# Kernel tuning notes

Hardware: AMD Instinct MI355X
Metric: run time of the kernel (lower is better)

The kernel has to match this reference:

```python
import jax, jax.numpy as jnp
import numpy as np

N = 50000       # num nodes
F_IN = 256      # num_features
HID = 128       # num_hidden
E = 800000      # structural edges (no self loops)
E_KNN = 500000  # knn edges (no self loops)


def setup_inputs() -> dict:
    rng = np.random.default_rng(0)
    # loop-free random edges: col != row guaranteed
    row = rng.integers(0, N, E)
    col = (row + 1 + rng.integers(0, N - 1, E)) % N
    edge_index = jnp.asarray(np.stack([row, col]), dtype=jnp.int32)
    rowk = rng.integers(0, N, E_KNN)
    colk = (rowk + 1 + rng.integers(0, N - 1, E_KNN)) % N
    knn_graph = jnp.asarray(np.stack([rowk, colk]), dtype=jnp.int32)

    key = jax.random.key(0)
    ks = jax.random.split(key, 8)
    x = jax.random.normal(ks[0], (N, F_IN), dtype=jnp.float32)
    s = 1.0 / np.sqrt(F_IN)  # nn.Linear default init range
    def lin(kw, kb):
        W = jax.random.uniform(kw, (HID, F_IN), minval=-s, maxval=s, dtype=jnp.float32)
        b = jax.random.uniform(kb, (HID,), minval=-s, maxval=s, dtype=jnp.float32)
        return W, b
    W_s1, b_s1 = lin(ks[1], ks[2])
    W_s2, b_s2 = lin(ks[3], ks[4])
    W_f2, b_f2 = lin(ks[5], ks[6])
    return {"x": x, "edge_index": edge_index, "knn_graph": knn_graph,
            "W_s1": W_s1, "b_s1": b_s1, "W_s2": W_s2, "b_s2": b_s2,
            "W_f2": W_f2, "b_f2": b_f2}


def _gcn_norm(edge_index, num_nodes):
    # add_remaining_self_loops on loop-free input == append all self loops (w=1)
    loop = jnp.arange(num_nodes, dtype=edge_index.dtype)
    row = jnp.concatenate([edge_index[0], loop])
    col = jnp.concatenate([edge_index[1], loop])
    w = jnp.ones(row.shape[0], dtype=jnp.float32)
    deg = jax.ops.segment_sum(w, col, num_segments=num_nodes)
    dinv = jnp.where(deg > 0, jax.lax.rsqrt(deg), 0.0)
    return row, col, dinv[row] * w * dinv[col]


def _gcn(x, W, b, row, col, norm, K):
    # eval mode: dropout(p=0.6) is identity
    h = x @ W.T + b
    n = x.shape[0]
    for _ in range(K):
        # gather source feats -> edge-weight scale -> scatter-add to targets (SpMM)
        h = jax.ops.segment_sum(norm[:, None] * h[row], col, num_segments=n)
    return h


def reference(x, edge_index, knn_graph, W_s1, b_s1, W_s2, b_s2, W_f2, b_f2):
    n = x.shape[0]
    r, c, nm = _gcn_norm(edge_index, n)
    rk, ck, nmk = _gcn_norm(knn_graph, n)
    h0 = _gcn(x, W_s1, b_s1, r, c, nm, 2)
    h1 = _gcn(x, W_s2, b_s2, r, c, nm, 10)
    z0 = _gcn(x, W_f2, b_f2, r, c, nm, 2)
    # original computes gcn_f2(x, edge_index, K=2) twice; in eval mode both equal z0
    z1 = z0 + _gcn(x, W_f2, b_f2, rk, ck, nmk, 1)
    return (h0, h1, z0, z1)
```

## Files before the change

kernel.cpp:

```cpp
#include <hip/hip_runtime.h>
#include <hip/hip_fp16.h>

#define F_IN 256
#define HID 128

typedef _Float16 half8 __attribute__((ext_vector_type(8)));
typedef _Float16 half4v __attribute__((ext_vector_type(4)));
typedef float f32x4 __attribute__((ext_vector_type(4)));


__global__ void k_count2(const int* __restrict__ col_s, int E, int* __restrict__ cnt_s,
                         const int* __restrict__ col_k, int EK, int* __restrict__ cnt_k) {
  int e = blockIdx.x * blockDim.x + threadIdx.x;
  if (e < E) {
    atomicAdd(&cnt_s[col_s[e]], 1);
  } else {
    int f = e - E;
    if (f < EK) atomicAdd(&cnt_k[col_k[f]], 1);
  }
}

__global__ void k_scan_block(const int* __restrict__ in, int n, int* __restrict__ out,
                             int* __restrict__ bsum) {
  __shared__ int s[1024];
  int tid = threadIdx.x;
  int i = blockIdx.x * 1024 + tid;
  int v = (i < n) ? in[i] : 0;
  s[tid] = v;
  __syncthreads();
  for (int off = 1; off < 1024; off <<= 1) {
    int t = (tid >= off) ? s[tid - off] : 0;
    __syncthreads();
    s[tid] += t;
    __syncthreads();
  }
  if (i < n) out[i] = s[tid] - v;
  if (tid == 1023) bsum[blockIdx.x] = s[1023];
}

__global__ void k_scan_single(int* __restrict__ bsum, int nb, int* __restrict__ tail) {
  if (threadIdx.x == 0 && blockIdx.x == 0) {
    int run = 0;
    for (int b = 0; b < nb; ++b) { int t = bsum[b]; bsum[b] = run; run += t; }
    *tail = run;
  }
}

__global__ void k_add_off(int* __restrict__ out, const int* __restrict__ bsum, int n) {
  int i = blockIdx.x * blockDim.x + threadIdx.x;
  if (i < n) out[i] += bsum[i >> 10];
}

__global__ void k_scatter2(const int* __restrict__ row_s, const int* __restrict__ col_s, int E,
                           const int* __restrict__ offs_s, int* __restrict__ cur_s,
                           int* __restrict__ csr_s,
                           const int* __restrict__ row_k, const int* __restrict__ col_k, int EK,
                           const int* __restrict__ offs_k, int* __restrict__ cur_k,
                           int* __restrict__ csr_k) {
  int e = blockIdx.x * blockDim.x + threadIdx.x;
  if (e < E) {
    int c = col_s[e];
    int p = offs_s[c] + atomicAdd(&cur_s[c], 1);
    csr_s[p] = row_s[e];
  } else {
    int f = e - E;
    if (f < EK) {
      int c = col_k[f];
      int p = offs_k[c] + atomicAdd(&cur_k[c], 1);
      csr_k[p] = row_k[f];
    }
  }
}


__global__ void k_cvt_w(const float* __restrict__ W0, const float* __restrict__ W1,
                        const float* __restrict__ W2, _Float16* __restrict__ Wh) {
  const int sz = HID * F_IN;
  int idx = (blockIdx.x * 256 + threadIdx.x) * 4;
  const float* src = (idx < sz) ? (W0 + idx)
                   : (idx < 2 * sz) ? (W1 + idx - sz)
                   : (W2 + idx - 2 * sz);
  float4 v = *(const float4*)src;
  half4v o;
  o[0] = (_Float16)v.x; o[1] = (_Float16)v.y; o[2] = (_Float16)v.z; o[3] = (_Float16)v.w;
  *(half4v*)(Wh + idx) = o;
}


__global__ __launch_bounds__(256, 8) void k_gemm3(
    const float* __restrict__ x, const _Float16* __restrict__ Wh,
    const float* __restrict__ b0, const float* __restrict__ b1, const float* __restrict__ b2,
    int n, const int* __restrict__ cnt_s, const int* __restrict__ cnt_k,
    _Float16* __restrict__ gS1, _Float16* __restrict__ gS2,
    _Float16* __restrict__ gF2s, _Float16* __restrict__ gF2k)
{
  __shared__ _Float16 xs[32 * F_IN];
  int tid = threadIdx.x;
  int m0 = blockIdx.x * 32;

  {
    int r = tid >> 3;
    int cbase = (tid & 7) * 32;
    int gr = m0 + r; if (gr >= n) gr = n - 1;
    const float* src = x + (size_t)gr * F_IN + cbase;
    unsigned sw = (unsigned)((r & 7) << 4);
    char* drow = (char*)xs + r * (F_IN * 2);
#pragma unroll
    for (int i = 0; i < 4; ++i) {
      float4 a = *(const float4*)(src + i * 8);
      float4 b = *(const float4*)(src + i * 8 + 4);
      half8 v;
      v[0] = (_Float16)a.x; v[1] = (_Float16)a.y; v[2] = (_Float16)a.z; v[3] = (_Float16)a.w;
      v[4] = (_Float16)b.x; v[5] = (_Float16)b.y; v[6] = (_Float16)b.z; v[7] = (_Float16)b.w;
      *(half8*)(drow + (((unsigned)(cbase * 2 + i * 16)) ^ sw)) = v;
    }
  }
  __syncthreads();

  int lane = tid & 63;
  int wv = tid >> 6;
  int mh = wv >> 1, ch = wv & 1;
  int l15 = lane & 15, lhi = lane >> 4;
  int rloc = mh * 16 + l15;
  unsigned swr = (unsigned)((rloc & 7) << 4);
  const char* xrow = (const char*)xs + rloc * (F_IN * 2);

  int node = m0 + rloc;
  int cn = (node < n) ? node : (n - 1);
  float ss = rsqrtf((float)(cnt_s[cn] + 1));
  float sk = rsqrtf((float)(cnt_k[cn] + 1));

#pragma unroll 1
  for (int w = 0; w < 3; ++w) {
    const float* bias = (w == 0) ? b0 : (w == 1) ? b1 : b2;
    _Float16* dst = (w == 0) ? gS1 : (w == 1) ? gS2 : gF2s;
    const _Float16* Wp = Wh + (size_t)w * HID * F_IN
                            + (size_t)(ch * 64 + l15) * F_IN + lhi * 8;

    f32x4 acc[4];
#pragma unroll
    for (int nt = 0; nt < 4; ++nt) {
      float4 bv = *(const float4*)(bias + ch * 64 + nt * 16 + lhi * 4);
      acc[nt] = (f32x4){bv.x, bv.y, bv.z, bv.w};
    }

#pragma unroll
    for (int kt = 0; kt < 8; ++kt) {
      half8 xf = *(const half8*)(xrow + (((unsigned)((kt * 32 + lhi * 8) * 2)) ^ swr));
#pragma unroll
      for (int nt = 0; nt < 4; ++nt) {
        half8 wf = *(const half8*)(Wp + (size_t)nt * 16 * F_IN + kt * 32);
        acc[nt] = __builtin_amdgcn_mfma_f32_16x16x32_f16(wf, xf, acc[nt], 0, 0, 0);
      }
    }

    if (node < n) {
      size_t obase = (size_t)node * HID + ch * 64 + lhi * 4;
#pragma unroll
      for (int nt = 0; nt < 4; ++nt) {
        half4v o;
        o[0] = (_Float16)(acc[nt][0] * ss); o[1] = (_Float16)(acc[nt][1] * ss);
        o[2] = (_Float16)(acc[nt][2] * ss); o[3] = (_Float16)(acc[nt][3] * ss);
        *(half4v*)(dst + obase + nt * 16) = o;
      }
      if (w == 2) {
#pragma unroll
        for (int nt = 0; nt < 4; ++nt) {
          half4v o2;
          o2[0] = (_Float16)(acc[nt][0] * sk); o2[1] = (_Float16)(acc[nt][1] * sk);
          o2[2] = (_Float16)(acc[nt][2] * sk); o2[3] = (_Float16)(acc[nt][3] * sk);
          *(half4v*)(gF2k + obase + nt * 16) = o2;
        }
      }
    }
  }
}


__device__ inline float2 h2f2(unsigned int u) {
  __half2 h; *(unsigned int*)&h = u; return __half22float2(h);
}

__device__ inline void spmm_store(void* out, size_t base, float2 acc, float deg, int mode,
                                  const float2* __restrict__ add) {
  if (mode == 0) {
    float sc = 1.0f / deg;
    __half2 h = __float22half2_rn(make_float2(acc.x * sc, acc.y * sc));
    ((__half2*)out)[base] = h;
  } else {
    float sc = rsqrtf(deg);
    float2 o = make_float2(acc.x * sc, acc.y * sc);
    if (mode == 2) { float2 z = add[base]; o.x += z.x; o.y += z.y; }
    ((float2*)out)[base] = o;
  }
}

__global__ __launch_bounds__(256) void k_spmm_h(
    const unsigned int* __restrict__ gin, void* __restrict__ gout,
    const int* __restrict__ csr, const int* __restrict__ offs, const int* __restrict__ cnt,
    int n, int mode, const float2* __restrict__ addsrc)
{
  int w = (blockIdx.x << 2) | ((int)threadIdx.x >> 6);
  if (w >= n) return;
  int lane = threadIdx.x & 63;
  int beg = offs[w], end = offs[w + 1];
  size_t base = (size_t)w * 64 + lane;
  float2 acc = h2f2(gin[base]);
  int e = beg;
#pragma unroll 1
  for (; e + 16 <= end; e += 16) {
    unsigned int u[16];
#pragma unroll
    for (int j = 0; j < 16; ++j)
      u[j] = gin[((size_t)(unsigned)csr[e + j] << 6) + lane];
    float sx = 0.f, sy = 0.f;
#pragma unroll
    for (int j = 0; j < 16; ++j) { float2 v = h2f2(u[j]); sx += v.x; sy += v.y; }
    acc.x += sx; acc.y += sy;
  }
#pragma unroll 1
  for (; e + 4 <= end; e += 4) {
    unsigned int u[4];
#pragma unroll
    for (int j = 0; j < 4; ++j)
      u[j] = gin[((size_t)(unsigned)csr[e + j] << 6) + lane];
    float sx = 0.f, sy = 0.f;
#pragma unroll
    for (int j = 0; j < 4; ++j) { float2 v = h2f2(u[j]); sx += v.x; sy += v.y; }
    acc.x += sx; acc.y += sy;
  }
  for (; e < end; ++e) {
    float2 v = h2f2(gin[((size_t)(unsigned)csr[e] << 6) + lane]);
    acc.x += v.x; acc.y += v.y;
  }
  spmm_store(gout, base, acc, (float)(cnt[w] + 1), mode, addsrc);
}

__global__ __launch_bounds__(256) void k_spmm3(
    const unsigned int* __restrict__ g0, const unsigned int* __restrict__ g1,
    const unsigned int* __restrict__ g2,
    void* __restrict__ o0, void* __restrict__ o1, void* __restrict__ o2,
    int md0, int md1, int md2,
    const int* __restrict__ csr, const int* __restrict__ offs, const int* __restrict__ cnt,
    int n)
{
  int w = (blockIdx.x << 2) | ((int)threadIdx.x >> 6);
  if (w >= n) return;
  int lane = threadIdx.x & 63;
  int beg = offs[w], end = offs[w + 1];
  size_t base = (size_t)w * 64 + lane;
  float2 a0 = h2f2(g0[base]), a1 = h2f2(g1[base]), a2 = h2f2(g2[base]);
  int e = beg;
#pragma unroll 1
  for (; e + 4 <= end; e += 4) {
    size_t s[4];
#pragma unroll
    for (int j = 0; j < 4; ++j) s[j] = ((size_t)(unsigned)csr[e + j] << 6) + lane;
    unsigned int u0[4], u1[4], u2[4];
#pragma unroll
    for (int j = 0; j < 4; ++j) { u0[j] = g0[s[j]]; u1[j] = g1[s[j]]; u2[j] = g2[s[j]]; }
#pragma unroll
    for (int j = 0; j < 4; ++j) {
      float2 v;
      v = h2f2(u0[j]); a0.x += v.x; a0.y += v.y;
      v = h2f2(u1[j]); a1.x += v.x; a1.y += v.y;
      v = h2f2(u2[j]); a2.x += v.x; a2.y += v.y;
    }
  }
  for (; e < end; ++e) {
    size_t s0 = ((size_t)(unsigned)csr[e] << 6) + lane;
    float2 v;
    v = h2f2(g0[s0]); a0.x += v.x; a0.y += v.y;
    v = h2f2(g1[s0]); a1.x += v.x; a1.y += v.y;
    v = h2f2(g2[s0]); a2.x += v.x; a2.y += v.y;
  }
  float deg = (float)(cnt[w] + 1);
  spmm_store(o0, base, a0, deg, md0, nullptr);
  spmm_store(o1, base, a1, deg, md1, nullptr);
  spmm_store(o2, base, a2, deg, md2, nullptr);
}


extern "C" void kernel_launch(void* const* d_in, const int* in_sizes, int n_in,
                              void* d_out, int out_size, void* d_ws, size_t ws_size,
                              hipStream_t stream) {
  const float* x    = (const float*)d_in[0];
  const int*   ei   = (const int*)d_in[1];
  const int*   knn  = (const int*)d_in[2];
  const float* W_s1 = (const float*)d_in[3];
  const float* b_s1 = (const float*)d_in[4];
  const float* W_s2 = (const float*)d_in[5];
  const float* b_s2 = (const float*)d_in[6];
  const float* W_f2 = (const float*)d_in[7];
  const float* b_f2 = (const float*)d_in[8];

  const int N  = in_sizes[0] / F_IN;
  const int E  = in_sizes[1] / 2;
  const int EK = in_sizes[2] / 2;
  const int* row_s = ei;   const int* col_s = ei + E;
  const int* row_k = knn;  const int* col_k = knn + EK;

  char* p = (char*)d_ws;
  auto carve = [&](size_t bytes) {
    char* r = p; p += (bytes + 511) & ~(size_t)511; return (void*)r;
  };
  int* cnt_s = (int*)carve((size_t)N * 4);
  int* cnt_k = (int*)carve((size_t)N * 4);
  int* cur_s = (int*)carve((size_t)N * 4);
  int* cur_k = (int*)carve((size_t)N * 4);
  char* zero_end = p;
  int* offs_s = (int*)carve((size_t)(N + 1) * 4);
  int* offs_k = (int*)carve((size_t)(N + 1) * 4);
  int* bsum   = (int*)carve(4096);
  int* csr_s  = (int*)carve((size_t)E * 4);
  int* csr_k  = (int*)carve((size_t)EK * 4);
  _Float16* Wh  = (_Float16*)carve((size_t)3 * HID * F_IN * 2);
  _Float16* gS1 = (_Float16*)carve((size_t)N * HID * 2);
  _Float16* gS2 = (_Float16*)carve((size_t)N * HID * 2);
  _Float16* gF2s= (_Float16*)carve((size_t)N * HID * 2);
  _Float16* gF2k= (_Float16*)carve((size_t)N * HID * 2);
  _Float16* tS2 = (_Float16*)carve((size_t)N * HID * 2);

  float* out_h0 = (float*)d_out;
  float* out_h1 = out_h0 + (size_t)N * HID;
  float* out_z0 = out_h1 + (size_t)N * HID;
  float* out_z1 = out_z0 + (size_t)N * HID;
  _Float16* tS1 = (_Float16*)out_z1;
  _Float16* tF2 = tS1 + (size_t)N * HID;

  hipMemsetAsync(d_ws, 0, (size_t)(zero_end - (char*)d_ws), stream);

  const int tpb = 256;
  int etot = E + EK;
  k_count2<<<(etot + tpb - 1) / tpb, tpb, 0, stream>>>(col_s, E, cnt_s, col_k, EK, cnt_k);

  int nb = (N + 1023) / 1024;
  k_scan_block<<<nb, 1024, 0, stream>>>(cnt_s, N, offs_s, bsum);
  k_scan_single<<<1, 64, 0, stream>>>(bsum, nb, offs_s + N);
  k_add_off<<<(N + tpb - 1) / tpb, tpb, 0, stream>>>(offs_s, bsum, N);
  k_scan_block<<<nb, 1024, 0, stream>>>(cnt_k, N, offs_k, bsum);
  k_scan_single<<<1, 64, 0, stream>>>(bsum, nb, offs_k + N);
  k_add_off<<<(N + tpb - 1) / tpb, tpb, 0, stream>>>(offs_k, bsum, N);

  k_scatter2<<<(etot + tpb - 1) / tpb, tpb, 0, stream>>>(
      row_s, col_s, E, offs_s, cur_s, csr_s,
      row_k, col_k, EK, offs_k, cur_k, csr_k);

  k_cvt_w<<<96, 256, 0, stream>>>(W_s1, W_s2, W_f2, Wh);
  k_gemm3<<<(N + 31) / 32, 256, 0, stream>>>(x, Wh, b_s1, b_s2, b_f2, N, cnt_s, cnt_k,
                                             gS1, gS2, gF2s, gF2k);

  int spmm_grid = (N + 3) / 4;

  k_spmm3<<<spmm_grid, 256, 0, stream>>>((const unsigned int*)gS1, (const unsigned int*)gS2,
                                         (const unsigned int*)gF2s,
                                         tS1, tS2, tF2, 0, 0, 0,
                                         csr_s, offs_s, cnt_s, N);
  k_spmm3<<<spmm_grid, 256, 0, stream>>>((const unsigned int*)tS1, (const unsigned int*)tS2,
                                         (const unsigned int*)tF2,
                                         out_h0, gS1, out_z0, 1, 0, 1,
                                         csr_s, offs_s, cnt_s, N);

  {
    _Float16* cur = gS1; _Float16* alt = tS2;
    for (int it = 0; it < 7; ++it) {
      k_spmm_h<<<spmm_grid, 256, 0, stream>>>((const unsigned int*)cur, alt,
                                              csr_s, offs_s, cnt_s, N, 0, nullptr);
      _Float16* t = cur; cur = alt; alt = t;
    }
    k_spmm_h<<<spmm_grid, 256, 0, stream>>>((const unsigned int*)cur, out_h1,
                                            csr_s, offs_s, cnt_s, N, 1, nullptr);
  }

  k_spmm_h<<<spmm_grid, 256, 0, stream>>>((const unsigned int*)gF2k, out_z1,
                                          csr_k, offs_k, cnt_k, N, 2,
                                          (const float2*)out_z0);
}
```

Measured before the change: 725.8 us.

## Vectorize SpMM gathers with 16-byte loads and split edges across lane groups

The SpMM kernels change lane mapping: each wavefront now splits into four 16-lane groups, each handling a different neighbor edge and loading 16 bytes (8 halfs) per lane instead of 4 bytes. Partial sums are combined with cross-group shuffles and only group 0 writes. The aim is fewer, wider memory transactions and more edges in flight per wave. The GEMM kernel also gains software prefetching of the next k-step's fragments and a lower launch-bounds occupancy hint. The costs are extra shuffle reductions, higher register pressure, and idle lanes on the final partial batch of edges.

```diff
diff --git a/kernel.cpp b/kernel.cpp
--- a/kernel.cpp
+++ b/kernel.cpp
@@ -7,6 +7,7 @@
 typedef _Float16 half8 __attribute__((ext_vector_type(8)));
 typedef _Float16 half4v __attribute__((ext_vector_type(4)));
 typedef float f32x4 __attribute__((ext_vector_type(4)));
+typedef unsigned int uint4v __attribute__((ext_vector_type(4)));
 
 
 __global__ void k_count2(const int* __restrict__ col_s, int E, int* __restrict__ cnt_s,
@@ -87,7 +88,7 @@
 }
 
 
-__global__ __launch_bounds__(256, 8) void k_gemm3(
+__global__ __launch_bounds__(256, 6) void k_gemm3(
     const float* __restrict__ x, const _Float16* __restrict__ Wh,
     const float* __restrict__ b0, const float* __restrict__ b1, const float* __restrict__ b2,
     int n, const int* __restrict__ cnt_s, const int* __restrict__ cnt_k,
@@ -144,13 +145,28 @@
       acc[nt] = (f32x4){bv.x, bv.y, bv.z, bv.w};
     }
 
+    half8 xf = *(const half8*)(xrow + (((unsigned)((0 * 32 + lhi * 8) * 2)) ^ swr));
+    half8 wf[4];
+#pragma unroll
+    for (int nt = 0; nt < 4; ++nt)
+      wf[nt] = *(const half8*)(Wp + (size_t)nt * 16 * F_IN + 0 * 32);
+
 #pragma unroll
     for (int kt = 0; kt < 8; ++kt) {
-      half8 xf = *(const half8*)(xrow + (((unsigned)((kt * 32 + lhi * 8) * 2)) ^ swr));
-#pragma unroll
-      for (int nt = 0; nt < 4; ++nt) {
-        half8 wf = *(const half8*)(Wp + (size_t)nt * 16 * F_IN + kt * 32);
-        acc[nt] = __builtin_amdgcn_mfma_f32_16x16x32_f16(wf, xf, acc[nt], 0, 0, 0);
+      half8 xfn; half8 wfn[4];
+      if (kt < 7) {
+        xfn = *(const half8*)(xrow + (((unsigned)(((kt + 1) * 32 + lhi * 8) * 2)) ^ swr));
+#pragma unroll
+        for (int nt = 0; nt < 4; ++nt)
+          wfn[nt] = *(const half8*)(Wp + (size_t)nt * 16 * F_IN + (kt + 1) * 32);
+      }
+#pragma unroll
+      for (int nt = 0; nt < 4; ++nt)
+        acc[nt] = __builtin_amdgcn_mfma_f32_16x16x32_f16(wf[nt], xf, acc[nt], 0, 0, 0);
+      if (kt < 7) {
+        xf = xfn;
+#pragma unroll
+        for (int nt = 0; nt < 4; ++nt) wf[nt] = wfn[nt];
       }
     }
 
@@ -181,64 +197,111 @@
   __half2 h; *(unsigned int*)&h = u; return __half22float2(h);
 }
 
-__device__ inline void spmm_store(void* out, size_t base, float2 acc, float deg, int mode,
-                                  const float2* __restrict__ add) {
-  if (mode == 0) {
-    float sc = 1.0f / deg;
-    __half2 h = __float22half2_rn(make_float2(acc.x * sc, acc.y * sc));
-    ((__half2*)out)[base] = h;
-  } else {
-    float sc = rsqrtf(deg);
-    float2 o = make_float2(acc.x * sc, acc.y * sc);
-    if (mode == 2) { float2 z = add[base]; o.x += z.x; o.y += z.y; }
-    ((float2*)out)[base] = o;
-  }
-}
-
 __global__ __launch_bounds__(256) void k_spmm_h(
-    const unsigned int* __restrict__ gin, void* __restrict__ gout,
+    const _Float16* __restrict__ gin, void* __restrict__ gout,
     const int* __restrict__ csr, const int* __restrict__ offs, const int* __restrict__ cnt,
-    int n, int mode, const float2* __restrict__ addsrc)
+    int n, int mode, const float* __restrict__ addsrc)
 {
   int w = (blockIdx.x << 2) | ((int)threadIdx.x >> 6);
   if (w >= n) return;
   int lane = threadIdx.x & 63;
+  int g = lane >> 4;
+  int c = lane & 15;
   int beg = offs[w], end = offs[w + 1];
-  size_t base = (size_t)w * 64 + lane;
-  float2 acc = h2f2(gin[base]);
+
+  float acc[8];
+#pragma unroll
+  for (int i = 0; i < 8; ++i) acc[i] = 0.f;
+
   int e = beg;
 #pragma unroll 1
   for (; e + 16 <= end; e += 16) {
-    unsigned int u[16];
-#pragma unroll
-    for (int j = 0; j < 16; ++j)
-      u[j] = gin[((size_t)(unsigned)csr[e + j] << 6) + lane];
-    float sx = 0.f, sy = 0.f;
-#pragma unroll
-    for (int j = 0; j < 16; ++j) { float2 v = h2f2(u[j]); sx += v.x; sy += v.y; }
-    acc.x += sx; acc.y += sy;
+    int idx[4];
+#pragma unroll
+    for (int j = 0; j < 4; ++j) idx[j] = csr[e + 4 * j + g];
+    uint4v u[4];
+#pragma unroll
+    for (int j = 0; j < 4; ++j)
+      u[j] = *(const uint4v*)(gin + ((size_t)(unsigned)idx[j] << 7) + c * 8);
+#pragma unroll
+    for (int j = 0; j < 4; ++j)
+#pragma unroll
+      for (int q = 0; q < 4; ++q) {
+        float2 v = h2f2(u[j][q]);
+        acc[q * 2] += v.x; acc[q * 2 + 1] += v.y;
+      }
   }
 #pragma unroll 1
   for (; e + 4 <= end; e += 4) {
-    unsigned int u[4];
-#pragma unroll
-    for (int j = 0; j < 4; ++j)
-      u[j] = gin[((size_t)(unsigned)csr[e + j] << 6) + lane];
-    float sx = 0.f, sy = 0.f;
-#pragma unroll
-    for (int j = 0; j < 4; ++j) { float2 v = h2f2(u[j]); sx += v.x; sy += v.y; }
-    acc.x += sx; acc.y += sy;
-  }
-  for (; e < end; ++e) {
-    float2 v = h2f2(gin[((size_t)(unsigned)csr[e] << 6) + lane]);
-    acc.x += v.x; acc.y += v.y;
-  }
-  spmm_store(gout, base, acc, (float)(cnt[w] + 1), mode, addsrc);
+    int idx = csr[e + g];
+    uint4v u = *(const uint4v*)(gin + ((size_t)(unsigned)idx << 7) + c * 8);
+#pragma unroll
+    for (int q = 0; q < 4; ++q) {
+      float2 v = h2f2(u[q]);
+      acc[q * 2] += v.x; acc[q * 2 + 1] += v.y;
+    }
+  }
+  {
+    int rem = end - e;
+    if (g < rem) {
+      int idx = csr[e + g];
+      uint4v u = *(const uint4v*)(gin + ((size_t)(unsigned)idx << 7) + c * 8);
+#pragma unroll
+      for (int q = 0; q < 4; ++q) {
+        float2 v = h2f2(u[q]);
+        acc[q * 2] += v.x; acc[q * 2 + 1] += v.y;
+      }
+    }
+  }
+#pragma unroll
+  for (int i = 0; i < 8; ++i) {
+    acc[i] += __shfl_xor(acc[i], 16, 64);
+    acc[i] += __shfl_xor(acc[i], 32, 64);
+  }
+  {
+    uint4v u = *(const uint4v*)(gin + ((size_t)w << 7) + c * 8);
+#pragma unroll
+    for (int q = 0; q < 4; ++q) {
+      float2 v = h2f2(u[q]);
+      acc[q * 2] += v.x; acc[q * 2 + 1] += v.y;
+    }
+  }
+
+  float deg = (float)(cnt[w] + 1);
+  if (mode == 0) {
+    float sc = 1.0f / deg;
+    if (g == 0) {
+      uint4v o;
+#pragma unroll
+      for (int q = 0; q < 4; ++q) {
+        __half2 h = __float22half2_rn(make_float2(acc[q * 2] * sc, acc[q * 2 + 1] * sc));
+        o[q] = *(unsigned int*)&h;
+      }
+      *(uint4v*)((_Float16*)gout + ((size_t)w << 7) + c * 8) = o;
+    }
+  } else {
+    float sc = rsqrtf(deg);
+    if (g == 0) {
+      float o[8];
+#pragma unroll
+      for (int i = 0; i < 8; ++i) o[i] = acc[i] * sc;
+      if (mode == 2) {
+        const float* ap = addsrc + ((size_t)w << 7) + c * 8;
+        float4 a0 = *(const float4*)ap;
+        float4 a1 = *(const float4*)(ap + 4);
+        o[0] += a0.x; o[1] += a0.y; o[2] += a0.z; o[3] += a0.w;
+        o[4] += a1.x; o[5] += a1.y; o[6] += a1.z; o[7] += a1.w;
+      }
+      float* op = (float*)gout + ((size_t)w << 7) + c * 8;
+      *(float4*)op = make_float4(o[0], o[1], o[2], o[3]);
+      *(float4*)(op + 4) = make_float4(o[4], o[5], o[6], o[7]);
+    }
+  }
 }
 
 __global__ __launch_bounds__(256) void k_spmm3(
-    const unsigned int* __restrict__ g0, const unsigned int* __restrict__ g1,
-    const unsigned int* __restrict__ g2,
+    const _Float16* __restrict__ g0, const _Float16* __restrict__ g1,
+    const _Float16* __restrict__ g2,
     void* __restrict__ o0, void* __restrict__ o1, void* __restrict__ o2,
     int md0, int md1, int md2,
     const int* __restrict__ csr, const int* __restrict__ offs, const int* __restrict__ cnt,
@@ -247,37 +310,117 @@
   int w = (blockIdx.x << 2) | ((int)threadIdx.x >> 6);
   if (w >= n) return;
   int lane = threadIdx.x & 63;
+  int g = lane >> 4;
+  int c = lane & 15;
   int beg = offs[w], end = offs[w + 1];
-  size_t base = (size_t)w * 64 + lane;
-  float2 a0 = h2f2(g0[base]), a1 = h2f2(g1[base]), a2 = h2f2(g2[base]);
+
+  float a0[8], a1[8], a2[8];
+#pragma unroll
+  for (int i = 0; i < 8; ++i) { a0[i] = 0.f; a1[i] = 0.f; a2[i] = 0.f; }
+
   int e = beg;
 #pragma unroll 1
   for (; e + 4 <= end; e += 4) {
-    size_t s[4];
-#pragma unroll
-    for (int j = 0; j < 4; ++j) s[j] = ((size_t)(unsigned)csr[e + j] << 6) + lane;
-    unsigned int u0[4], u1[4], u2[4];
-#pragma unroll
-    for (int j = 0; j < 4; ++j) { u0[j] = g0[s[j]]; u1[j] = g1[s[j]]; u2[j] = g2[s[j]]; }
-#pragma unroll
-    for (int j = 0; j < 4; ++j) {
+    size_t off = ((size_t)(unsigned)csr[e + g] << 7) + c * 8;
+    uint4v u0 = *(const uint4v*)(g0 + off);
+    uint4v u1 = *(const uint4v*)(g1 + off);
+    uint4v u2 = *(const uint4v*)(g2 + off);
+#pragma unroll
+    for (int q = 0; q < 4; ++q) {
       float2 v;
-      v = h2f2(u0[j]); a0.x += v.x; a0.y += v.y;
-      v = h2f2(u1[j]); a1.x += v.x; a1.y += v.y;
-      v = h2f2(u2[j]); a2.x += v.x; a2.y += v.y;
-    }
-  }
-  for (; e < end; ++e) {
-    size_t s0 = ((size_t)(unsigned)csr[e] << 6) + lane;
-    float2 v;
-    v = h2f2(g0[s0]); a0.x += v.x; a0.y += v.y;
-    v = h2f2(g1[s0]); a1.x += v.x; a1.y += v.y;
-    v = h2f2(g2[s0]); a2.x += v.x; a2.y += v.y;
-  }
+      v = h2f2(u0[q]); a0[q * 2] += v.x; a0[q * 2 + 1] += v.y;
+      v = h2f2(u1[q]); a1[q * 2] += v.x; a1[q * 2 + 1] += v.y;
+      v = h2f2(u2[q]); a2[q * 2] += v.x; a2[q * 2 + 1] += v.y;
+    }
+  }
+  {
+    int rem = end - e;
+    if (g < rem) {
+      size_t off = ((size_t)(unsigned)csr[e + g] << 7) + c * 8;
+      uint4v u0 = *(const uint4v*)(g0 + off);
+      uint4v u1 = *(const uint4v*)(g1 + off);
+      uint4v u2 = *(const uint4v*)(g2 + off);
+#pragma unroll
+      for (int q = 0; q < 4; ++q) {
+        float2 v;
+        v = h2f2(u0[q]); a0[q * 2] += v.x; a0[q * 2 + 1] += v.y;
+        v = h2f2(u1[q]); a1[q * 2] += v.x; a1[q * 2 + 1] += v.y;
+        v = h2f2(u2[q]); a2[q * 2] += v.x; a2[q * 2 + 1] += v.y;
+      }
+    }
+  }
+#pragma unroll
+  for (int i = 0; i < 8; ++i) {
+    a0[i] += __shfl_xor(a0[i], 16, 64); a0[i] += __shfl_xor(a0[i], 32, 64);
+    a1[i] += __shfl_xor(a1[i], 16, 64); a1[i] += __shfl_xor(a1[i], 32, 64);
+    a2[i] += __shfl_xor(a2[i], 16, 64); a2[i] += __shfl_xor(a2[i], 32, 64);
+  }
+  {
+    size_t off = ((size_t)w << 7) + c * 8;
+    uint4v u0 = *(const uint4v*)(g0 + off);
+    uint4v u1 = *(const uint4v*)(g1 + off);
+    uint4v u2 = *(const uint4v*)(g2 + off);
+#pragma unroll
+    for (int q = 0; q < 4; ++q) {
+      float2 v;
+      v = h2f2(u0[q]); a0[q * 2] += v.x; a0[q * 2 + 1] += v.y;
+      v = h2f2(u1[q]); a1[q * 2] += v.x; a1[q * 2 + 1] += v.y;
+      v = h2f2(u2[q]); a2[q * 2] += v.x; a2[q * 2 + 1] += v.y;
+    }
+  }
+
   float deg = (float)(cnt[w] + 1);
-  spmm_store(o0, base, a0, deg, md0, nullptr);
-  spmm_store(o1, base, a1, deg, md1, nullptr);
-  spmm_store(o2, base, a2, deg, md2, nullptr);
+  if (g == 0) {
+    float inv = 1.0f / deg, rs = rsqrtf(deg);
+    {
+      float sc = (md0 == 0) ? inv : rs;
+      if (md0 == 0) {
+        uint4v o;
+#pragma unroll
+        for (int q = 0; q < 4; ++q) {
+          __half2 h = __float22half2_rn(make_float2(a0[q * 2] * sc, a0[q * 2 + 1] * sc));
+          o[q] = *(unsigned int*)&h;
+        }
+        *(uint4v*)((_Float16*)o0 + ((size_t)w << 7) + c * 8) = o;
+      } else {
+        float* op = (float*)o0 + ((size_t)w << 7) + c * 8;
+        *(float4*)op = make_float4(a0[0] * sc, a0[1] * sc, a0[2] * sc, a0[3] * sc);
+        *(float4*)(op + 4) = make_float4(a0[4] * sc, a0[5] * sc, a0[6] * sc, a0[7] * sc);
+      }
+    }
+    {
+      float sc = (md1 == 0) ? inv : rs;
+      if (md1 == 0) {
+        uint4v o;
+#pragma unroll
+        for (int q = 0; q < 4; ++q) {
+          __half2 h = __float22half2_rn(make_float2(a1[q * 2] * sc, a1[q * 2 + 1] * sc));
+          o[q] = *(unsigned int*)&h;
+        }
+        *(uint4v*)((_Float16*)o1 + ((size_t)w << 7) + c * 8) = o;
+      } else {
+        float* op = (float*)o1 + ((size_t)w << 7) + c * 8;
+        *(float4*)op = make_float4(a1[0] * sc, a1[1] * sc, a1[2] * sc, a1[3] * sc);
+        *(float4*)(op + 4) = make_float4(a1[4] * sc, a1[5] * sc, a1[6] * sc, a1[7] * sc);
+      }
+    }
+    {
+      float sc = (md2 == 0) ? inv : rs;
+      if (md2 == 0) {
+        uint4v o;
+#pragma unroll
+        for (int q = 0; q < 4; ++q) {
+          __half2 h = __float22half2_rn(make_float2(a2[q * 2] * sc, a2[q * 2 + 1] * sc));
+          o[q] = *(unsigned int*)&h;
+        }
+        *(uint4v*)((_Float16*)o2 + ((size_t)w << 7) + c * 8) = o;
+      } else {
+        float* op = (float*)o2 + ((size_t)w << 7) + c * 8;
+        *(float4*)op = make_float4(a2[0] * sc, a2[1] * sc, a2[2] * sc, a2[3] * sc);
+        *(float4*)(op + 4) = make_float4(a2[4] * sc, a2[5] * sc, a2[6] * sc, a2[7] * sc);
+      }
+    }
+  }
 }
 
 
@@ -352,27 +495,25 @@
 
   int spmm_grid = (N + 3) / 4;
 
-  k_spmm3<<<spmm_grid, 256, 0, stream>>>((const unsigned int*)gS1, (const unsigned int*)gS2,
-                                         (const unsigned int*)gF2s,
+  k_spmm3<<<spmm_grid, 256, 0, stream>>>(gS1, gS2, gF2s,
                                          tS1, tS2, tF2, 0, 0, 0,
                                          csr_s, offs_s, cnt_s, N);
-  k_spmm3<<<spmm_grid, 256, 0, stream>>>((const unsigned int*)tS1, (const unsigned int*)tS2,
-                                         (const unsigned int*)tF2,
+  k_spmm3<<<spmm_grid, 256, 0, stream>>>(tS1, tS2, tF2,
                                          out_h0, gS1, out_z0, 1, 0, 1,
                                          csr_s, offs_s, cnt_s, N);
 
   {
     _Float16* cur = gS1; _Float16* alt = tS2;
     for (int it = 0; it < 7; ++it) {
-      k_spmm_h<<<spmm_grid, 256, 0, stream>>>((const unsigned int*)cur, alt,
+      k_spmm_h<<<spmm_grid, 256, 0, stream>>>(cur, alt,
                                               csr_s, offs_s, cnt_s, N, 0, nullptr);
       _Float16* t = cur; cur = alt; alt = t;
     }
-    k_spmm_h<<<spmm_grid, 256, 0, stream>>>((const unsigned int*)cur, out_h1,
+    k_spmm_h<<<spmm_grid, 256, 0, stream>>>(cur, out_h1,
                                             csr_s, offs_s, cnt_s, N, 1, nullptr);
   }
 
-  k_spmm_h<<<spmm_grid, 256, 0, stream>>>((const unsigned int*)gF2k, out_z1,
+  k_spmm_h<<<spmm_grid, 256, 0, stream>>>(gF2k, out_z1,
                                           csr_k, offs_k, cnt_k, N, 2,
-                                          (const float2*)out_z0);
-}
+                                          out_z0);
+}
```

Result: no change. 713.6 us (-1.7%).
